# Performance work log

Hardware: AMD Instinct MI355X
Metric: run time of the kernel (lower is better)

The kernel has to match this reference:

```python
import jax, jax.numpy as jnp
import numpy as np

N_NODES = 100000
N_EDGES = 1600000
IN_F = 128
H_F = 128
N_CLS = 8
N_LAYERS = 6


def setup_inputs() -> dict:
    key = jax.random.key(0)
    ks = jax.random.split(key, 8)
    scale = 1.0 / np.sqrt(H_F)
    return {
        "in_feat": jax.random.normal(ks[0], (N_NODES, IN_F), dtype=jnp.float32),
        "src": jax.random.randint(ks[1], (N_EDGES,), 0, N_NODES, dtype=jnp.int32),
        "dst": jax.random.randint(ks[2], (N_EDGES,), 0, N_NODES, dtype=jnp.int32),
        "edge_weight": jax.random.uniform(ks[3], (N_EDGES,), dtype=jnp.float32),
        "conv_W": jax.random.normal(ks[4], (N_LAYERS, H_F, H_F), dtype=jnp.float32) * scale,
        "conv_b": jnp.zeros((N_LAYERS, H_F), dtype=jnp.float32),
        "lin_W": jax.random.normal(ks[5], (H_F, N_CLS), dtype=jnp.float32) * scale,
        "lin_b": jnp.zeros((N_CLS,), dtype=jnp.float32),
    }


def _degree_norms(src, dst, n):
    ones = jnp.ones(src.shape[0], dtype=jnp.float32)
    out_deg = jax.ops.segment_sum(ones, src, num_segments=n)
    in_deg = jax.ops.segment_sum(ones, dst, num_segments=n)
    # DGL norm='both': clamp degrees to min 1, then ^-0.5 (structural degrees)
    norm_src = jnp.power(jnp.maximum(out_deg, 1.0), -0.5)[:, None]  # [N,1]
    norm_dst = jnp.power(jnp.maximum(in_deg, 1.0), -0.5)[:, None]   # [N,1]
    return norm_src, norm_dst


def _graph_conv(x, W, b, src, dst, ew, norm_src, norm_dst):
    # linear commutes with (linear) aggregation; apply weight first
    h = (x @ W) * norm_src                     # [N,F]
    msg = h[src] * ew[:, None]                 # [E,F] gather * edge weight
    agg = jax.ops.segment_sum(msg, dst, num_segments=x.shape[0])
    return agg * norm_dst + b


def reference(in_feat, src, dst, edge_weight, conv_W, conv_b, lin_W, lin_b):
    norm_src, norm_dst = _degree_norms(src, dst, in_feat.shape[0])
    h = in_feat
    for i in range(N_LAYERS):
        h = jax.nn.leaky_relu(
            _graph_conv(h, conv_W[i], conv_b[i], src, dst, edge_weight, norm_src, norm_dst),
            negative_slope=0.01,
        )
    return h @ lin_W + lin_b
```

## Files before the change

### kernel.cpp

```cpp
#include <hip/hip_runtime.h>
#include <math.h>

#define N_NODES 100000
#define N_EDGES 1600000
#define HF 128
#define N_CLS 8
#define N_LAYERS 6
#define TILE_N 64
#define SCAN_B 1024
#define SCAN_NB ((N_NODES + SCAN_B - 1) / SCAN_B)
#define HBINS 8192
#define HCHUNK ((N_NODES + HBINS - 1) / HBINS)
#define HSLICE 8

typedef __attribute__((ext_vector_type(8))) short bf16x8;
typedef __attribute__((ext_vector_type(4))) float f32x4;

__device__ __forceinline__ unsigned short bf_rne(float x) {
    unsigned u = __float_as_uint(x);
    u += 0x7FFFu + ((u >> 16) & 1u);
    return (unsigned short)(u >> 16);
}
__device__ __forceinline__ float bf_to_f(unsigned short h) {
    return __uint_as_float(((unsigned)h) << 16);
}

#define LDSOFF(row, k) (((row) << 8) + (((((k) >> 3) << 4) ^ (((row) & 7) << 4))) + (((k) & 7) << 1))

__global__ void deg_rank_kernel(const int* __restrict__ dst,
                                int* __restrict__ ind, int* __restrict__ rank) {
    int e = blockIdx.x * blockDim.x + threadIdx.x;
    if (e < N_EDGES) {
        rank[e] = atomicAdd(&ind[dst[e]], 1);
    }
}

__global__ __launch_bounds__(1024) void outdeg_hist_kernel(const int* __restrict__ src,
                                                           int* __restrict__ outd) {
    __shared__ int hist[HBINS];
    int chunk = blockIdx.x;
    int slice = blockIdx.y;
    int lo = chunk * HBINS;
    int hi = lo + HBINS;
    for (int i = threadIdx.x; i < HBINS; i += 1024) hist[i] = 0;
    __syncthreads();
    const int4* s4 = (const int4*)src;
    const int n4 = N_EDGES / 4;
    int per = (n4 + HSLICE - 1) / HSLICE;
    int beg = slice * per;
    int end = beg + per; if (end > n4) end = n4;
    for (int i = beg + threadIdx.x; i < end; i += 1024) {
        int4 v = s4[i];
        if (v.x >= lo && v.x < hi) atomicAdd(&hist[v.x - lo], 1);
        if (v.y >= lo && v.y < hi) atomicAdd(&hist[v.y - lo], 1);
        if (v.z >= lo && v.z < hi) atomicAdd(&hist[v.z - lo], 1);
        if (v.w >= lo && v.w < hi) atomicAdd(&hist[v.w - lo], 1);
    }
    __syncthreads();
    for (int i = threadIdx.x; i < HBINS; i += 1024) {
        int c = hist[i];
        if (c != 0 && lo + i < N_NODES) atomicAdd(&outd[lo + i], c);
    }
}

__global__ void norm_kernel(const int* __restrict__ outd, const int* __restrict__ ind,
                            float* __restrict__ ns, float* __restrict__ nd) {
    int n = blockIdx.x * blockDim.x + threadIdx.x;
    if (n < N_NODES) {
        int od = outd[n]; if (od < 1) od = 1;
        int id = ind[n];  if (id < 1) id = 1;
        ns[n] = rsqrtf((float)od);
        nd[n] = rsqrtf((float)id);
    }
}

__global__ __launch_bounds__(SCAN_B) void scan1_kernel(const int* __restrict__ deg,
                                                       int* __restrict__ incl,
                                                       int* __restrict__ bsum) {
    __shared__ int buf[SCAN_B];
    int t = threadIdx.x;
    int g = blockIdx.x * SCAN_B + t;
    int v = (g < N_NODES) ? deg[g] : 0;
    buf[t] = v;
    __syncthreads();
    #pragma unroll
    for (int off = 1; off < SCAN_B; off <<= 1) {
        int add = (t >= off) ? buf[t - off] : 0;
        __syncthreads();
        buf[t] += add;
        __syncthreads();
    }
    if (g < N_NODES) incl[g] = buf[t];
    if (t == SCAN_B - 1) bsum[blockIdx.x] = buf[t];
}

__global__ __launch_bounds__(128) void scan2_kernel(int* __restrict__ bsum) {
    __shared__ int buf[128];
    int t = threadIdx.x;
    buf[t] = (t < SCAN_NB) ? bsum[t] : 0;
    __syncthreads();
    #pragma unroll
    for (int off = 1; off < 128; off <<= 1) {
        int add = (t >= off) ? buf[t - off] : 0;
        __syncthreads();
        buf[t] += add;
        __syncthreads();
    }
    if (t < SCAN_NB) bsum[t] = buf[t];
}

__global__ __launch_bounds__(SCAN_B) void scan3_kernel(const int* __restrict__ deg,
                                                       const int* __restrict__ incl,
                                                       const int* __restrict__ bsum,
                                                       int* __restrict__ row_ptr) {
    int t = threadIdx.x;
    int g = blockIdx.x * SCAN_B + t;
    if (g < N_NODES) {
        int off = (blockIdx.x > 0) ? bsum[blockIdx.x - 1] : 0;
        row_ptr[g] = off + incl[g] - deg[g];
    }
    if (g == 0) row_ptr[N_NODES] = bsum[SCAN_NB - 1];
}

__global__ void scatter2_kernel(const int* __restrict__ src, const int* __restrict__ dst,
                                const float* __restrict__ ew, const float* __restrict__ ns,
                                const float* __restrict__ nd, const int* __restrict__ row_ptr,
                                const int* __restrict__ rank, float2* __restrict__ esw) {
    int e = blockIdx.x * blockDim.x + threadIdx.x;
    if (e < N_EDGES) {
        int s = src[e];
        int d = dst[e];
        int pos = row_ptr[d] + rank[e];
        esw[pos] = make_float2(__int_as_float(s), ew[e] * ns[s] * nd[d]);
    }
}

__global__ __launch_bounds__(256) void wprep_kernel(const float* __restrict__ conv_W,
                                                    unsigned short* __restrict__ wt) {
    int l = blockIdx.y;
    int idx = blockIdx.x * 256 + threadIdx.x;
    int k = idx >> 7, f = idx & 127;
    float x = conv_W[(size_t)l * 16384 + idx];
    unsigned short h0 = bf_rne(x);
    float r1 = x - bf_to_f(h0);
    unsigned short h1 = bf_rne(r1);
    float r2 = r1 - bf_to_f(h1);
    unsigned short h2 = bf_rne(r2);
    size_t base = (size_t)l * 3 * 16384 + (size_t)f * 128 + k;
    wt[base]         = h0;
    wt[base + 16384] = h1;
    wt[base + 32768] = h2;
}

__global__ __launch_bounds__(256) void gemm_mfma_kernel(const float* __restrict__ X,
                                                        const unsigned short* __restrict__ Wt,
                                                        float* __restrict__ Y) {
    __shared__ unsigned short Xb[3][TILE_N * HF];
    int tid = threadIdx.x;
    int nodeBase = blockIdx.x * TILE_N;

    for (int it = 0; it < 8; it++) {
        int idx = tid + it * 256;
        int r = idx >> 5;
        int c = idx & 31;
        int n = nodeBase + r;
        float4 v = make_float4(0.f, 0.f, 0.f, 0.f);
        if (n < N_NODES) v = ((const float4*)(X + (size_t)n * HF))[c];
        float vv[4] = {v.x, v.y, v.z, v.w};
        unsigned short h0[4], h1[4], h2[4];
        #pragma unroll
        for (int j = 0; j < 4; j++) {
            float x = vv[j];
            h0[j] = bf_rne(x);
            float r1 = x - bf_to_f(h0[j]);
            h1[j] = bf_rne(r1);
            float r2 = r1 - bf_to_f(h1[j]);
            h2[j] = bf_rne(r2);
        }
        int boff = LDSOFF(r, c * 4) >> 1;
        *(uint2*)&Xb[0][boff] = *(uint2*)h0;
        *(uint2*)&Xb[1][boff] = *(uint2*)h1;
        *(uint2*)&Xb[2][boff] = *(uint2*)h2;
    }
    __syncthreads();

    int lane = tid & 63;
    int wv = tid >> 6;
    int lrow = lane & 15;
    int lk8 = lane >> 4;

    f32x4 acc[4][2];
    #pragma unroll
    for (int m = 0; m < 4; m++)
        #pragma unroll
        for (int n = 0; n < 2; n++)
            acc[m][n] = (f32x4){0.f, 0.f, 0.f, 0.f};

    const int pa[6] = {0, 0, 1, 0, 1, 2};
    const int pb[6] = {0, 1, 0, 2, 1, 0};

    #pragma unroll
    for (int p = 0; p < 6; p++) {
        const unsigned short* xb = Xb[pa[p]];
        const unsigned short* wb = Wt + (size_t)pb[p] * 16384;
        #pragma unroll
        for (int ks = 0; ks < 4; ks++) {
            int k0 = ks * 32 + lk8 * 8;
            bf16x8 afr[4];
            #pragma unroll
            for (int m = 0; m < 4; m++) {
                int row = m * 16 + lrow;
                afr[m] = *(const bf16x8*)&xb[LDSOFF(row, k0) >> 1];
            }
            bf16x8 bfr[2];
            #pragma unroll
            for (int n = 0; n < 2; n++) {
                int col = wv * 32 + n * 16 + lrow;
                bfr[n] = *(const bf16x8*)&wb[col * 128 + k0];
            }
            #pragma unroll
            for (int m = 0; m < 4; m++)
                #pragma unroll
                for (int n = 0; n < 2; n++)
                    acc[m][n] = __builtin_amdgcn_mfma_f32_16x16x32_bf16(
                        afr[m], bfr[n], acc[m][n], 0, 0, 0);
        }
    }

    #pragma unroll
    for (int m = 0; m < 4; m++) {
        int rowBase = nodeBase + m * 16 + lk8 * 4;
        #pragma unroll
        for (int n = 0; n < 2; n++) {
            int feat = wv * 32 + n * 16 + lrow;
            #pragma unroll
            for (int rr = 0; rr < 4; rr++) {
                int nd = rowBase + rr;
                if (nd < N_NODES) Y[(size_t)nd * HF + feat] = acc[m][n][rr];
            }
        }
    }
}

__global__ __launch_bounds__(256) void agg_kernel(const float* __restrict__ hl,
                                                  const int* __restrict__ row_ptr,
                                                  const float2* __restrict__ esw,
                                                  const float* __restrict__ bias,
                                                  float* __restrict__ out) {
    int node = blockIdx.x * 4 + (threadIdx.x >> 6);
    if (node >= N_NODES) return;
    int lane = threadIdx.x & 63;
    int half = lane >> 5;
    int fl = lane & 31;

    int beg = row_ptr[node];
    int end = row_ptr[node + 1];
    float ax = 0.f, ay = 0.f, az = 0.f, aw = 0.f;

    int i = beg;
    for (; i + 2 <= end; i += 2) {
        float2 p = esw[i + half];
        int s = __float_as_int(p.x);
        float4 v = ((const float4*)(hl + (size_t)s * HF))[fl];
        ax += v.x * p.y; ay += v.y * p.y;
        az += v.z * p.y; aw += v.w * p.y;
    }
    if (i < end && half == 0) {
        float2 p = esw[i];
        int s = __float_as_int(p.x);
        float4 v = ((const float4*)(hl + (size_t)s * HF))[fl];
        ax += v.x * p.y; ay += v.y * p.y;
        az += v.z * p.y; aw += v.w * p.y;
    }

    ax += __shfl_xor(ax, 32);
    ay += __shfl_xor(ay, 32);
    az += __shfl_xor(az, 32);
    aw += __shfl_xor(aw, 32);

    if (half == 0) {
        float4 bb = ((const float4*)bias)[fl];
        float ox = ax + bb.x;
        float oy = ay + bb.y;
        float oz = az + bb.z;
        float ow = aw + bb.w;
        ox = (ox > 0.f) ? ox : 0.01f * ox;
        oy = (oy > 0.f) ? oy : 0.01f * oy;
        oz = (oz > 0.f) ? oz : 0.01f * oz;
        ow = (ow > 0.f) ? ow : 0.01f * ow;
        ((float4*)(out + (size_t)node * HF))[fl] = make_float4(ox, oy, oz, ow);
    }
}

__global__ __launch_bounds__(256) void proj_kernel(const float* __restrict__ h,
                                                   const float* __restrict__ W,
                                                   const float* __restrict__ b,
                                                   float* __restrict__ out) {
    int node = blockIdx.x * (blockDim.x >> 6) + (threadIdx.x >> 6);
    if (node >= N_NODES) return;
    int lane = threadIdx.x & 63;

    float2 v = *(const float2*)(h + (size_t)node * HF + lane * 2);
    float acc[N_CLS];
    #pragma unroll
    for (int c = 0; c < N_CLS; c++) {
        acc[c] = v.x * W[(lane * 2) * N_CLS + c] + v.y * W[(lane * 2 + 1) * N_CLS + c];
    }
    #pragma unroll
    for (int off = 32; off > 0; off >>= 1) {
        #pragma unroll
        for (int c = 0; c < N_CLS; c++) acc[c] += __shfl_down(acc[c], off);
    }
    if (lane == 0) {
        #pragma unroll
        for (int c = 0; c < N_CLS; c++) out[(size_t)node * N_CLS + c] = acc[c] + b[c];
    }
}

extern "C" void kernel_launch(void* const* d_in, const int* in_sizes, int n_in,
                              void* d_out, int out_size, void* d_ws, size_t ws_size,
                              hipStream_t stream) {
    const float* in_feat = (const float*)d_in[0];
    const int*   src     = (const int*)d_in[1];
    const int*   dst     = (const int*)d_in[2];
    const float* ew      = (const float*)d_in[3];
    const float* conv_W  = (const float*)d_in[4];
    const float* conv_b  = (const float*)d_in[5];
    const float* lin_W   = (const float*)d_in[6];
    const float* lin_b   = (const float*)d_in[7];
    float* out = (float*)d_out;

    char* p = (char*)d_ws;
    float* hA = (float*)p;        p += (size_t)N_NODES * HF * sizeof(float);
    float* hB = (float*)p;        p += (size_t)N_NODES * HF * sizeof(float);
    float2* esw = (float2*)p;     p += (size_t)N_EDGES * sizeof(float2);
    int*   row_ptr = (int*)p;     p += ((size_t)N_NODES + 8) * sizeof(int);
    int*   out_deg = (int*)p;     p += (size_t)N_NODES * sizeof(int);
    int*   in_deg = (int*)p;      p += (size_t)N_NODES * sizeof(int);
    float* norm_src = (float*)p;  p += (size_t)N_NODES * sizeof(float);
    float* norm_dst = (float*)p;  p += (size_t)N_NODES * sizeof(float);
    int*   incl = (int*)p;        p += (size_t)N_NODES * sizeof(int);
    int*   bsum = (int*)p;        p += 256 * sizeof(int);
    unsigned short* wt = (unsigned short*)p; p += (size_t)N_LAYERS * 3 * 16384 * sizeof(unsigned short);
    int*   rank = (int*)hB;
    (void)p; (void)ws_size; (void)in_sizes; (void)n_in; (void)out_size;

    hipMemsetAsync(out_deg, 0, (size_t)N_NODES * sizeof(int), stream);
    hipMemsetAsync(in_deg, 0, (size_t)N_NODES * sizeof(int), stream);

    int egrid = (N_EDGES + 255) / 256;
    int ngrid = (N_NODES + 255) / 256;

    deg_rank_kernel<<<egrid, 256, 0, stream>>>(dst, in_deg, rank);
    outdeg_hist_kernel<<<dim3(HCHUNK, HSLICE), 1024, 0, stream>>>(src, out_deg);
    norm_kernel<<<ngrid, 256, 0, stream>>>(out_deg, in_deg, norm_src, norm_dst);
    scan1_kernel<<<SCAN_NB, SCAN_B, 0, stream>>>(in_deg, incl, bsum);
    scan2_kernel<<<1, 128, 0, stream>>>(bsum);
    scan3_kernel<<<SCAN_NB, SCAN_B, 0, stream>>>(in_deg, incl, bsum, row_ptr);
    scatter2_kernel<<<egrid, 256, 0, stream>>>(src, dst, ew, norm_src, norm_dst,
                                               row_ptr, rank, esw);
    wprep_kernel<<<dim3(64, N_LAYERS), 256, 0, stream>>>(conv_W, wt);

    int ggrid = (N_NODES + TILE_N - 1) / TILE_N;
    int agrid = (N_NODES + 3) / 4;

    const float* cur = in_feat;
    for (int l = 0; l < N_LAYERS; l++) {
        gemm_mfma_kernel<<<ggrid, 256, 0, stream>>>(cur, wt + (size_t)l * 3 * 16384, hB);
        agg_kernel<<<agrid, 256, 0, stream>>>(hB, row_ptr, esw,
                                              conv_b + (size_t)l * HF, hA);
        cur = hA;
    }
    proj_kernel<<<agrid, 256, 0, stream>>>(hA, lin_W, lin_b, out);
}
```

Baseline: 1.364 ms.

## Fuse neighbor aggregation and MFMA transform into one per-layer kernel

Each layer now runs one kernel instead of two. It aggregates the weighted neighbor features of 32 nodes into LDS as split-bf16 parts, then applies the layer weights with MFMA, adds bias and applies leaky ReLU. This relies on the linear map commuting with aggregation, and it removes the write and re-read of the full intermediate feature matrix plus one launch per layer. In exchange each wave aggregates 8 nodes one after another before the GEMM, which may reduce memory-level parallelism for the gather. Output buffers now alternate between layers.

After: 2.344 ms. +71.9%, slower.

```diff
diff --git a/kernel.cpp b/kernel.cpp
--- a/kernel.cpp
+++ b/kernel.cpp
@@ -6,7 +6,7 @@
 #define HF 128
 #define N_CLS 8
 #define N_LAYERS 6
-#define TILE_N 64
+#define TILE_M 32
 #define SCAN_B 1024
 #define SCAN_NB ((N_NODES + SCAN_B - 1) / SCAN_B)
 #define HBINS 8192
@@ -152,46 +152,69 @@
     wt[base + 32768] = h2;
 }
 
-__global__ __launch_bounds__(256) void gemm_mfma_kernel(const float* __restrict__ X,
-                                                        const unsigned short* __restrict__ Wt,
-                                                        float* __restrict__ Y) {
-    __shared__ unsigned short Xb[3][TILE_N * HF];
+__global__ __launch_bounds__(256) void fused_layer_kernel(
+        const float* __restrict__ hl, const int* __restrict__ row_ptr,
+        const float2* __restrict__ esw, const unsigned short* __restrict__ Wt,
+        const float* __restrict__ bias, float* __restrict__ out) {
+    __shared__ unsigned short Xb[3][TILE_M * HF];
     int tid = threadIdx.x;
-    int nodeBase = blockIdx.x * TILE_N;
-
-    for (int it = 0; it < 8; it++) {
-        int idx = tid + it * 256;
-        int r = idx >> 5;
-        int c = idx & 31;
-        int n = nodeBase + r;
-        float4 v = make_float4(0.f, 0.f, 0.f, 0.f);
-        if (n < N_NODES) v = ((const float4*)(X + (size_t)n * HF))[c];
-        float vv[4] = {v.x, v.y, v.z, v.w};
+    int nodeBase = blockIdx.x * TILE_M;
+    int wv = tid >> 6;
+    int lane = tid & 63;
+    int half = lane >> 5;
+    int fl = lane & 31;
+
+    for (int idx = 0; idx < 8; idx++) {
+        int lr = wv * 8 + idx;
+        int node = nodeBase + lr;
+        int beg = row_ptr[node];
+        int end = row_ptr[node + 1];
+        float ax = 0.f, ay = 0.f, az = 0.f, aw = 0.f;
+        int i = beg;
+        for (; i + 2 <= end; i += 2) {
+            float2 p = esw[i + half];
+            int s = __float_as_int(p.x);
+            float4 v = ((const float4*)(hl + (size_t)s * HF))[fl];
+            ax += v.x * p.y; ay += v.y * p.y;
+            az += v.z * p.y; aw += v.w * p.y;
+        }
+        if (i < end && half == 0) {
+            float2 p = esw[i];
+            int s = __float_as_int(p.x);
+            float4 v = ((const float4*)(hl + (size_t)s * HF))[fl];
+            ax += v.x * p.y; ay += v.y * p.y;
+            az += v.z * p.y; aw += v.w * p.y;
+        }
+        ax += __shfl_xor(ax, 32);
+        ay += __shfl_xor(ay, 32);
+        az += __shfl_xor(az, 32);
+        aw += __shfl_xor(aw, 32);
+        float g[4] = {ax, ay, az, aw};
         unsigned short h0[4], h1[4], h2[4];
         #pragma unroll
         for (int j = 0; j < 4; j++) {
-            float x = vv[j];
-            h0[j] = bf_rne(x);
-            float r1 = x - bf_to_f(h0[j]);
+            h0[j] = bf_rne(g[j]);
+            float r1 = g[j] - bf_to_f(h0[j]);
             h1[j] = bf_rne(r1);
             float r2 = r1 - bf_to_f(h1[j]);
             h2[j] = bf_rne(r2);
         }
-        int boff = LDSOFF(r, c * 4) >> 1;
-        *(uint2*)&Xb[0][boff] = *(uint2*)h0;
-        *(uint2*)&Xb[1][boff] = *(uint2*)h1;
-        *(uint2*)&Xb[2][boff] = *(uint2*)h2;
-    }
-    __syncthreads();
-
-    int lane = tid & 63;
-    int wv = tid >> 6;
+        int boff = LDSOFF(lr, fl * 4) >> 1;
+        if (half == 0) {
+            *(uint2*)&Xb[0][boff] = *(uint2*)h0;
+            *(uint2*)&Xb[1][boff] = *(uint2*)h1;
+        } else {
+            *(uint2*)&Xb[2][boff] = *(uint2*)h2;
+        }
+    }
+    __syncthreads();
+
     int lrow = lane & 15;
     int lk8 = lane >> 4;
 
-    f32x4 acc[4][2];
-    #pragma unroll
-    for (int m = 0; m < 4; m++)
+    f32x4 acc[2][2];
+    #pragma unroll
+    for (int m = 0; m < 2; m++)
         #pragma unroll
         for (int n = 0; n < 2; n++)
             acc[m][n] = (f32x4){0.f, 0.f, 0.f, 0.f};
@@ -206,9 +229,9 @@
         #pragma unroll
         for (int ks = 0; ks < 4; ks++) {
             int k0 = ks * 32 + lk8 * 8;
-            bf16x8 afr[4];
+            bf16x8 afr[2];
             #pragma unroll
-            for (int m = 0; m < 4; m++) {
+            for (int m = 0; m < 2; m++) {
                 int row = m * 16 + lrow;
                 afr[m] = *(const bf16x8*)&xb[LDSOFF(row, k0) >> 1];
             }
@@ -219,7 +242,7 @@
                 bfr[n] = *(const bf16x8*)&wb[col * 128 + k0];
             }
             #pragma unroll
-            for (int m = 0; m < 4; m++)
+            for (int m = 0; m < 2; m++)
                 #pragma unroll
                 for (int n = 0; n < 2; n++)
                     acc[m][n] = __builtin_amdgcn_mfma_f32_16x16x32_bf16(
@@ -228,67 +251,19 @@
     }
 
     #pragma unroll
-    for (int m = 0; m < 4; m++) {
-        int rowBase = nodeBase + m * 16 + lk8 * 4;
-        #pragma unroll
-        for (int n = 0; n < 2; n++) {
-            int feat = wv * 32 + n * 16 + lrow;
+    for (int n = 0; n < 2; n++) {
+        int feat = wv * 32 + n * 16 + lrow;
+        float bb = bias[feat];
+        #pragma unroll
+        for (int m = 0; m < 2; m++) {
+            int rowBase = nodeBase + m * 16 + lk8 * 4;
             #pragma unroll
             for (int rr = 0; rr < 4; rr++) {
-                int nd = rowBase + rr;
-                if (nd < N_NODES) Y[(size_t)nd * HF + feat] = acc[m][n][rr];
+                float o = acc[m][n][rr] + bb;
+                o = (o > 0.f) ? o : 0.01f * o;
+                out[(size_t)(rowBase + rr) * HF + feat] = o;
             }
         }
-    }
-}
-
-__global__ __launch_bounds__(256) void agg_kernel(const float* __restrict__ hl,
-                                                  const int* __restrict__ row_ptr,
-                                                  const float2* __restrict__ esw,
-                                                  const float* __restrict__ bias,
-                                                  float* __restrict__ out) {
-    int node = blockIdx.x * 4 + (threadIdx.x >> 6);
-    if (node >= N_NODES) return;
-    int lane = threadIdx.x & 63;
-    int half = lane >> 5;
-    int fl = lane & 31;
-
-    int beg = row_ptr[node];
-    int end = row_ptr[node + 1];
-    float ax = 0.f, ay = 0.f, az = 0.f, aw = 0.f;
-
-    int i = beg;
-    for (; i + 2 <= end; i += 2) {
-        float2 p = esw[i + half];
-        int s = __float_as_int(p.x);
-        float4 v = ((const float4*)(hl + (size_t)s * HF))[fl];
-        ax += v.x * p.y; ay += v.y * p.y;
-        az += v.z * p.y; aw += v.w * p.y;
-    }
-    if (i < end && half == 0) {
-        float2 p = esw[i];
-        int s = __float_as_int(p.x);
-        float4 v = ((const float4*)(hl + (size_t)s * HF))[fl];
-        ax += v.x * p.y; ay += v.y * p.y;
-        az += v.z * p.y; aw += v.w * p.y;
-    }
-
-    ax += __shfl_xor(ax, 32);
-    ay += __shfl_xor(ay, 32);
-    az += __shfl_xor(az, 32);
-    aw += __shfl_xor(aw, 32);
-
-    if (half == 0) {
-        float4 bb = ((const float4*)bias)[fl];
-        float ox = ax + bb.x;
-        float oy = ay + bb.y;
-        float oz = az + bb.z;
-        float ow = aw + bb.w;
-        ox = (ox > 0.f) ? ox : 0.01f * ox;
-        oy = (oy > 0.f) ? oy : 0.01f * oy;
-        oz = (oz > 0.f) ? oz : 0.01f * oz;
-        ow = (ow > 0.f) ? ow : 0.01f * ow;
-        ((float4*)(out + (size_t)node * HF))[fl] = make_float4(ox, oy, oz, ow);
     }
 }
 
@@ -361,15 +336,16 @@
                                                row_ptr, rank, esw);
     wprep_kernel<<<dim3(64, N_LAYERS), 256, 0, stream>>>(conv_W, wt);
 
-    int ggrid = (N_NODES + TILE_N - 1) / TILE_N;
+    int fgrid = N_NODES / TILE_M;
     int agrid = (N_NODES + 3) / 4;
 
     const float* cur = in_feat;
     for (int l = 0; l < N_LAYERS; l++) {
-        gemm_mfma_kernel<<<ggrid, 256, 0, stream>>>(cur, wt + (size_t)l * 3 * 16384, hB);
-        agg_kernel<<<agrid, 256, 0, stream>>>(hB, row_ptr, esw,
-                                              conv_b + (size_t)l * HF, hA);
-        cur = hA;
+        float* nxt = (l & 1) ? hA : hB;
+        fused_layer_kernel<<<fgrid, 256, 0, stream>>>(cur, row_ptr, esw,
+                                                      wt + (size_t)l * 3 * 16384,
+                                                      conv_b + (size_t)l * HF, nxt);
+        cur = nxt;
     }
     proj_kernel<<<agrid, 256, 0, stream>>>(hA, lin_W, lin_b, out);
 }
```
